# Kernel tuning notes

Hardware: AMD Instinct MI355X
Metric: run time of the kernel (lower is better)

## Reference

```python
import jax, jax.numpy as jnp
import numpy as np

N_NODES = 100000
N_EDGES = 1250000
HID = 64          # structure_hidden_dim
N_RBF = 32
N_GRAPHS = 512
N_EXPERTS = 8
N_LAYERS = 3
CUTOFF = 6.0
MAX_Z = 100
GATE_IN = HID + N_EXPERTS  # 72
G1, G2 = 64, 32            # gate_hidden_dims


def setup_inputs() -> dict:
    key = jax.random.key(0)
    ks = jax.random.split(key, 32)
    s = 0.05
    inp = {
        'z': jax.random.randint(ks[0], (N_NODES,), 0, MAX_Z),
        'edge_index': jax.random.randint(ks[1], (2, N_EDGES), 0, N_NODES),
        'edge_weight': jax.random.uniform(ks[2], (N_EDGES,), dtype=jnp.float32) * CUTOFF,
        'batch': jnp.sort(jax.random.randint(ks[3], (N_NODES,), 0, N_GRAPHS)),
        'mlip_energies': jax.random.normal(ks[4], (N_GRAPHS, N_EXPERTS), dtype=jnp.float32),
        # SchNet parameters (torch nn.Linear convention: W is [out, in])
        'emb': jax.random.normal(ks[5], (MAX_Z, HID)) * s,
        'fW1': jax.random.normal(ks[6], (N_LAYERS, HID, N_RBF)) * s,
        'fb1': jnp.zeros((N_LAYERS, HID)),
        'fW2': jax.random.normal(ks[7], (N_LAYERS, HID, HID)) * s,
        'fb2': jnp.zeros((N_LAYERS, HID)),
        'dW': jax.random.normal(ks[8], (N_LAYERS, HID, HID)) * s,
        'db': jnp.zeros((N_LAYERS, HID)),
        'uW1': jax.random.normal(ks[9], (N_LAYERS, HID, HID)) * s,
        'ub1': jnp.zeros((N_LAYERS, HID)),
        'uW2': jax.random.normal(ks[10], (N_LAYERS, HID, HID)) * s,
        'ub2': jnp.zeros((N_LAYERS, HID)),
        # Gating MLP: (HID+E) -> 64 -> 32 -> E
        'gW1': jax.random.normal(ks[11], (G1, GATE_IN)) * s,
        'gb1': jnp.zeros((G1,)),
        'gW2': jax.random.normal(ks[12], (G2, G1)) * s,
        'gb2': jnp.zeros((G2,)),
        'gW3': jax.random.normal(ks[13], (N_EXPERTS, G2)) * s,
        'gb3': jnp.zeros((N_EXPERTS,)),
    }
    return inp


def reference(z, edge_index, edge_weight, batch, mlip_energies,
              emb, fW1, fb1, fW2, fb2, dW, db, uW1, ub1, uW2, ub2,
              gW1, gb1, gW2, gb2, gW3, gb3):
    src, dst = edge_index[0], edge_index[1]

    # Gaussian smearing of distances -> [E, N_RBF]
    offsets = jnp.linspace(0.0, CUTOFF, N_RBF, dtype=edge_weight.dtype)
    delta = offsets[1] - offsets[0]
    coeff = -0.5 / (delta * delta)
    diff = edge_weight[:, None] - offsets
    edge_attr = jnp.exp(coeff * diff * diff)

    # atom embedding [N, HID]
    x = emb[z]

    for i in range(N_LAYERS):
        # filter network: Linear -> SiLU -> Linear on RBF features [E, HID]
        f = jax.nn.silu(edge_attr @ fW1[i].T + fb1[i]) @ fW2[i].T + fb2[i]
        # gather + dense + elementwise filter -> messages [E, HID]
        msg = (x[src] @ dW[i].T + db[i]) * f
        # scatter-add to destination nodes [N, HID]
        agg = jax.ops.segment_sum(msg, dst, num_segments=N_NODES)
        # residual update MLP
        x = x + (jax.nn.silu(agg @ uW1[i].T + ub1[i]) @ uW2[i].T + ub2[i])

    # mean pool per graph [G, HID]
    pooled = jax.ops.segment_sum(x, batch, num_segments=N_GRAPHS)
    counts = jax.ops.segment_sum(jnp.ones((N_NODES,), x.dtype), batch, num_segments=N_GRAPHS)
    structure_embedding = pooled / jnp.maximum(counts, 1.0)[:, None]

    # gated MoE head
    gate_in = jnp.concatenate([structure_embedding, mlip_energies], axis=-1)
    h = jax.nn.relu(gate_in @ gW1.T + gb1)
    h = jax.nn.relu(h @ gW2.T + gb2)
    logits = h @ gW3.T + gb3
    weights = jax.nn.softmax(logits, axis=-1)
    prediction = jnp.sum(mlip_energies * weights, axis=-1)
    return (logits, weights, prediction)
```

## Files before the change

### kernel.cpp

```cpp
#include <hip/hip_runtime.h>
#include <hip/hip_fp16.h>
#include <math.h>

#define N_NODES   100000
#define N_EDGES   1250000
#define HID       64
#define N_RBF     32
#define N_GRAPHS  512
#define N_EXPERTS 8
#define N_LAYERS  3
#define CUTOFF    6.0f
#define GATE_IN   72
#define G1_DIM    64
#define G2_DIM    32
#define K_TAB     4096
#define N_BUCKET  391
#define BUCKET_CAP 4608
#define CHUNK_A   2048

typedef short short8 __attribute__((ext_vector_type(8)));
typedef float float4v __attribute__((ext_vector_type(4)));

__device__ __forceinline__ unsigned enc8(float v) {
  unsigned short u = __half_as_ushort(__float2half(v));
  return (unsigned)((unsigned short)(u + 0x80u) >> 8);
}
__device__ __forceinline__ float dec8(unsigned b) {
  return __half2float(__ushort_as_half((unsigned short)(b << 8)));
}
__device__ __forceinline__ unsigned short bf16(float f) {
  unsigned u = __float_as_uint(f);
  u += 0x7fffu + ((u >> 16) & 1u);
  return (unsigned short)(u >> 16);
}

__global__ __launch_bounds__(256) void build_tab(
    const float* __restrict__ fW1, const float* __restrict__ fb1,
    const float* __restrict__ fW2, const float* __restrict__ fb2,
    float* __restrict__ tab) {
  __shared__ float W1s[64][33];
  __shared__ float W2s[64][65];
  __shared__ float rbfs[4][32];
  __shared__ float h1s[4][64];
  int t = threadIdx.x;
  int wv = t >> 6, lane = t & 63;
  int layer = blockIdx.x / 1025;
  int k = (blockIdx.x % 1025) * 4 + wv;

  for (int i = t; i < 64 * 32; i += 256) W1s[i >> 5][i & 31] = fW1[layer * 2048 + i];
  for (int i = t; i < 64 * 64; i += 256) W2s[i >> 6][i & 63] = fW2[layer * 4096 + i];

  float w = (CUTOFF / (float)K_TAB) * (float)k;
  const float delta = CUTOFF / (float)(N_RBF - 1);
  const float coeff = -0.5f / (delta * delta);
  __syncthreads();

  if (lane < N_RBF) {
    float d = w - delta * (float)lane;
    rbfs[wv][lane] = expf(coeff * d * d);
  }
  __syncthreads();

  float s = fb1[layer * HID + lane];
#pragma unroll
  for (int j = 0; j < N_RBF; j++) s += rbfs[wv][j] * W1s[lane][j];
  h1s[wv][lane] = s / (1.0f + expf(-s));
  __syncthreads();

  float f = fb2[layer * HID + lane];
#pragma unroll
  for (int c = 0; c < HID; c++) f += h1s[wv][c] * W2s[lane][c];
  if (k <= K_TAB) tab[(layer * (K_TAB + 1) + k) * HID + lane] = f;
}

__global__ __launch_bounds__(256) void pack_tab8(
    const float* __restrict__ tab, unsigned char* __restrict__ tab8) {
  int i = blockIdx.x * 256 + threadIdx.x;
  if (i >= N_LAYERS * K_TAB * 64) return;
  int layer = i / (K_TAB * 64);
  int r = i - layer * (K_TAB * 64);
  const float* base = tab + layer * (K_TAB + 1) * 64;
  tab8[i] = (unsigned char)enc8(0.5f * (base[r] + base[r + 64]));
}

__global__ __launch_bounds__(256) void conv_w(
    const float* __restrict__ dW, const float* __restrict__ uW1,
    const float* __restrict__ uW2, unsigned short* __restrict__ dWh,
    unsigned short* __restrict__ uW1h, unsigned short* __restrict__ uW2h) {
  int i = blockIdx.x * 256 + threadIdx.x;
  if (i < N_LAYERS * 4096) {
    dWh[i]  = bf16(dW[i]);
    uW1h[i] = bf16(uW1[i]);
    uW2h[i] = bf16(uW2[i]);
  }
}

__global__ __launch_bounds__(256) void partitionA(
    const int* __restrict__ src, const int* __restrict__ dst,
    const float* __restrict__ ew, int* __restrict__ gcnt,
    uint2* __restrict__ stage) {
  __shared__ int hist[N_BUCKET];
  __shared__ int base[N_BUCKET];
  int t = threadIdx.x;
  int e0 = blockIdx.x * CHUNK_A;
  int e1 = e0 + CHUNK_A; if (e1 > N_EDGES) e1 = N_EDGES;

  for (int i = t; i < N_BUCKET; i += 256) hist[i] = 0;
  __syncthreads();
  for (int e = e0 + t; e < e1; e += 256)
    atomicAdd(&hist[dst[e] >> 8], 1);
  __syncthreads();
  for (int i = t; i < N_BUCKET; i += 256) {
    int c = hist[i];
    base[i] = c ? atomicAdd(&gcnt[i], c) : 0;
    hist[i] = 0;
  }
  __syncthreads();
  for (int e = e0 + t; e < e1; e += 256) {
    int d = dst[e];
    int b = d >> 8;
    int r = base[b] + atomicAdd(&hist[b], 1);
    if (r < BUCKET_CAP) {
      float uq = ew[e] * ((float)K_TAB / CUTOFF);
      int wq = (int)uq;
      if (wq > K_TAB - 1) wq = K_TAB - 1;
      stage[(size_t)b * BUCKET_CAP + r] =
          make_uint2(((unsigned)src[e] << 12) | (unsigned)wq, (unsigned)d);
    }
  }
}

__global__ __launch_bounds__(512) void bscan_kernel(
    const int* __restrict__ gcnt, int* __restrict__ bbase,
    int* __restrict__ rowstart) {
  __shared__ int sh[512];
  int t = threadIdx.x;
  int v = 0;
  if (t < N_BUCKET) {
    v = gcnt[t];
    if (v > BUCKET_CAP) v = BUCKET_CAP;
  }
  sh[t] = v;
  __syncthreads();
  for (int off = 1; off < 512; off <<= 1) {
    int add = (t >= off) ? sh[t - off] : 0;
    __syncthreads();
    sh[t] += add;
    __syncthreads();
  }
  if (t < N_BUCKET) bbase[t] = sh[t] - v;
  if (t == N_BUCKET - 1) {
    bbase[N_BUCKET] = sh[t];
    rowstart[N_NODES] = sh[t];
  }
}

__global__ __launch_bounds__(512) void sortB(
    const int* __restrict__ bbase, const uint2* __restrict__ stage,
    int* __restrict__ rowstart, unsigned* __restrict__ recs) {
  __shared__ int cnt[256];
  __shared__ int scn[256];
  __shared__ unsigned dest[BUCKET_CAP];
  int t = threadIdx.x;
  int b = blockIdx.x;
  int node0 = b << 8;
  int base = bbase[b];
  int total = bbase[b + 1] - base;
  const uint2* st = stage + (size_t)b * BUCKET_CAP;

  if (t < 256) cnt[t] = 0;
  __syncthreads();
  for (int k = t; k < total; k += 512) atomicAdd(&cnt[(int)st[k].y - node0], 1);
  __syncthreads();
  int v = 0;
  if (t < 256) { v = cnt[t]; scn[t] = v; }
  __syncthreads();
  for (int off = 1; off < 256; off <<= 1) {
    int add = (t < 256 && t >= off) ? scn[t - off] : 0;
    __syncthreads();
    if (t < 256) scn[t] += add;
    __syncthreads();
  }
  if (t < 256) {
    int excl = scn[t] - v;
    int n = node0 + t;
    if (n < N_NODES) rowstart[n] = base + excl;
    scn[t] = excl;
    cnt[t] = 0;
  }
  __syncthreads();
  for (int k = t; k < total; k += 512) {
    uint2 e = st[k];
    int ln = (int)e.y - node0;
    int r = atomicAdd(&cnt[ln], 1);
    dest[scn[ln] + r] = e.x;
  }
  __syncthreads();
  for (int k = t; k < total; k += 512) recs[base + k] = dest[k];
}

__global__ __launch_bounds__(256, 4) void dense0(
    const int* __restrict__ z, const float* __restrict__ emb,
    const unsigned short* __restrict__ Wh,
    const float* __restrict__ b, unsigned char* __restrict__ yb) {
  __shared__ __align__(16) unsigned char smem[18432];
  short* As = (short*)smem;
  short* Bs = As + 64 * 72;
  float* Es = (float*)smem;
  int t = threadIdx.x;
  int row0 = blockIdx.x * 64;

#pragma unroll
  for (int it = 0; it < 4; it++) {
    int i = it * 1024 + t * 4;
    int r = i >> 6, c = i & 63;
    int gr = row0 + r;
    float4 v = make_float4(0.f, 0.f, 0.f, 0.f);
    if (gr < N_NODES) {
      int zi = z[gr];
      v = *(const float4*)&emb[(size_t)zi * 64 + c];
    }
    short4 h;
    h.x = (short)bf16(v.x); h.y = (short)bf16(v.y);
    h.z = (short)bf16(v.z); h.w = (short)bf16(v.w);
    *(short4*)&As[r * 72 + c] = h;
  }
#pragma unroll
  for (int it = 0; it < 2; it++) {
    int i = it * 2048 + t * 8;
    int r = i >> 6, c = i & 63;
    *(uint4*)&Bs[r * 72 + c] = *(const uint4*)&Wh[i];
  }
  __syncthreads();

  int lane = t & 63, wv = t >> 6;
  int m = lane & 15, quad = lane >> 4;
  const short* arow = As + (wv * 16 + m) * 72 + quad * 8;
  short8 a0 = *(const short8*)arow;
  short8 a1 = *(const short8*)(arow + 32);
  float4v acc[4];
#pragma unroll
  for (int ct = 0; ct < 4; ct++) {
    const short* brow = Bs + (ct * 16 + m) * 72 + quad * 8;
    short8 bf0 = *(const short8*)brow;
    short8 bf1 = *(const short8*)(brow + 32);
    float bj = b[ct * 16 + m];
    float4v c = {bj, bj, bj, bj};
    c = __builtin_amdgcn_mfma_f32_16x16x32_bf16(a0, bf0, c, 0, 0, 0);
    c = __builtin_amdgcn_mfma_f32_16x16x32_bf16(a1, bf1, c, 0, 0, 0);
    acc[ct] = c;
  }
  __syncthreads();
#pragma unroll
  for (int ct = 0; ct < 4; ct++)
#pragma unroll
    for (int r = 0; r < 4; r++)
      Es[(wv * 16 + quad * 4 + r) * 68 + ct * 16 + m] = acc[ct][r];
  __syncthreads();
  {
    int row = t >> 2, c0 = (t & 3) * 16;
    int gr = row0 + row;
    if (gr < N_NODES) {
      unsigned w[4];
#pragma unroll
      for (int q = 0; q < 4; q++) {
        const float* p = &Es[row * 68 + c0 + 4 * q];
        w[q] = enc8(p[0]) | (enc8(p[1]) << 8) | (enc8(p[2]) << 16) | (enc8(p[3]) << 24);
      }
      *(uint4*)&yb[(size_t)gr * 64 + c0] = make_uint4(w[0], w[1], w[2], w[3]);
    }
  }
}

__global__ __launch_bounds__(256, 4) void update_dense(
    const unsigned short* __restrict__ aggb,
    const unsigned short* __restrict__ W1h, const float* __restrict__ ub1,
    const unsigned short* __restrict__ W2h, const float* __restrict__ ub2,
    float* __restrict__ x,
    const int* __restrict__ z, const float* __restrict__ emb,
    const unsigned short* __restrict__ dWn, const float* __restrict__ dbn,
    unsigned char* __restrict__ yb) {
  __shared__ __align__(16) short A1[64 * 72];
  __shared__ __align__(16) short B1[64 * 72];
  __shared__ __align__(16) float E[64 * 68];
  int t = threadIdx.x;
  int row0 = blockIdx.x * 64;
  int lane = t & 63, wv = t >> 6;
  int m = lane & 15, quad = lane >> 4;

#pragma unroll
  for (int it = 0; it < 4; it++) {
    int i = it * 1024 + t * 4;
    int r = i >> 6, c = i & 63;
    int gr = row0 + r;
    float4 v = make_float4(0.f, 0.f, 0.f, 0.f);
    if (gr < N_NODES) {
      if (z) {
        int zi = z[gr];
        v = *(const float4*)&emb[(size_t)zi * 64 + c];
      } else {
        v = *(const float4*)&x[(size_t)gr * 64 + c];
      }
    }
    *(float4*)&E[r * 68 + c] = v;
  }
#pragma unroll
  for (int it = 0; it < 2; it++) {
    int i = it * 2048 + t * 8;
    int r = i >> 6, c = i & 63;
    int gr = row0 + r;
    uint4 v = make_uint4(0u, 0u, 0u, 0u);
    if (gr < N_NODES) v = *(const uint4*)&aggb[(size_t)gr * 64 + c];
    *(uint4*)&A1[r * 72 + c] = v;
    *(uint4*)&B1[r * 72 + c] = *(const uint4*)&W1h[i];
  }
  __syncthreads();

  const short* arow = A1 + (wv * 16 + m) * 72 + quad * 8;
  float4v acc[4];
  {
    short8 a0 = *(const short8*)arow;
    short8 a1 = *(const short8*)(arow + 32);
#pragma unroll
    for (int ct = 0; ct < 4; ct++) {
      const short* brow = B1 + (ct * 16 + m) * 72 + quad * 8;
      short8 bf0 = *(const short8*)brow;
      short8 bf1 = *(const short8*)(brow + 32);
      float bj = ub1[ct * 16 + m];
      float4v c = {bj, bj, bj, bj};
      c = __builtin_amdgcn_mfma_f32_16x16x32_bf16(a0, bf0, c, 0, 0, 0);
      c = __builtin_amdgcn_mfma_f32_16x16x32_bf16(a1, bf1, c, 0, 0, 0);
      acc[ct] = c;
    }
  }
  __syncthreads();
#pragma unroll
  for (int ct = 0; ct < 4; ct++)
#pragma unroll
    for (int r = 0; r < 4; r++) {
      float s = acc[ct][r];
      float h = s / (1.0f + expf(-s));
      A1[(wv * 16 + quad * 4 + r) * 72 + ct * 16 + m] = (short)bf16(h);
    }
#pragma unroll
  for (int it = 0; it < 2; it++) {
    int i = it * 2048 + t * 8;
    int r = i >> 6, c = i & 63;
    *(uint4*)&B1[r * 72 + c] = *(const uint4*)&W2h[i];
  }
  __syncthreads();

  {
    short8 a0 = *(const short8*)arow;
    short8 a1 = *(const short8*)(arow + 32);
#pragma unroll
    for (int ct = 0; ct < 4; ct++) {
      const short* brow = B1 + (ct * 16 + m) * 72 + quad * 8;
      short8 bf0 = *(const short8*)brow;
      short8 bf1 = *(const short8*)(brow + 32);
      float bj = ub2[ct * 16 + m];
      float4v c = {bj, bj, bj, bj};
      c = __builtin_amdgcn_mfma_f32_16x16x32_bf16(a0, bf0, c, 0, 0, 0);
      c = __builtin_amdgcn_mfma_f32_16x16x32_bf16(a1, bf1, c, 0, 0, 0);
      acc[ct] = c;
    }
  }
  __syncthreads();
#pragma unroll
  for (int ct = 0; ct < 4; ct++)
#pragma unroll
    for (int r = 0; r < 4; r++)
      E[(wv * 16 + quad * 4 + r) * 68 + ct * 16 + m] += acc[ct][r];
  __syncthreads();
  {
    int row = t >> 2, c0 = (t & 3) * 16;
    int gr = row0 + row;
    if (gr < N_NODES) {
      float* xp = x + (size_t)gr * 64 + c0;
#pragma unroll
      for (int q = 0; q < 4; q++)
        *(float4*)(xp + 4 * q) = *(const float4*)&E[row * 68 + c0 + 4 * q];
    }
  }
  if (!dWn) return;

#pragma unroll
  for (int it = 0; it < 4; it++) {
    int i = it * 1024 + t * 4;
    int r = i >> 6, c = i & 63;
    float4 v = *(const float4*)&E[r * 68 + c];
    short4 h;
    h.x = (short)bf16(v.x); h.y = (short)bf16(v.y);
    h.z = (short)bf16(v.z); h.w = (short)bf16(v.w);
    *(short4*)&A1[r * 72 + c] = h;
  }
#pragma unroll
  for (int it = 0; it < 2; it++) {
    int i = it * 2048 + t * 8;
    int r = i >> 6, c = i & 63;
    *(uint4*)&B1[r * 72 + c] = *(const uint4*)&dWn[i];
  }
  __syncthreads();
  {
    short8 a0 = *(const short8*)arow;
    short8 a1 = *(const short8*)(arow + 32);
#pragma unroll
    for (int ct = 0; ct < 4; ct++) {
      const short* brow = B1 + (ct * 16 + m) * 72 + quad * 8;
      short8 bf0 = *(const short8*)brow;
      short8 bf1 = *(const short8*)(brow + 32);
      float bj = dbn[ct * 16 + m];
      float4v c = {bj, bj, bj, bj};
      c = __builtin_amdgcn_mfma_f32_16x16x32_bf16(a0, bf0, c, 0, 0, 0);
      c = __builtin_amdgcn_mfma_f32_16x16x32_bf16(a1, bf1, c, 0, 0, 0);
      acc[ct] = c;
    }
  }
  __syncthreads();
#pragma unroll
  for (int ct = 0; ct < 4; ct++)
#pragma unroll
    for (int r = 0; r < 4; r++)
      E[(wv * 16 + quad * 4 + r) * 68 + ct * 16 + m] = acc[ct][r];
  __syncthreads();
  {
    int row = t >> 2, c0 = (t & 3) * 16;
    int gr = row0 + row;
    if (gr < N_NODES) {
      unsigned w[4];
#pragma unroll
      for (int q = 0; q < 4; q++) {
        const float* p = &E[row * 68 + c0 + 4 * q];
        w[q] = enc8(p[0]) | (enc8(p[1]) << 8) | (enc8(p[2]) << 16) | (enc8(p[3]) << 24);
      }
      *(uint4*)&yb[(size_t)gr * 64 + c0] = make_uint4(w[0], w[1], w[2], w[3]);
    }
  }
}

__global__ __launch_bounds__(256) void gather_kernel(
    const int* __restrict__ rowstart, const unsigned* __restrict__ recs,
    const unsigned char* __restrict__ tab8,
    const unsigned char* __restrict__ yb,
    unsigned short* __restrict__ aggb) {
  int d = blockIdx.x * 4 + (threadIdx.x >> 6);
  int lane = threadIdx.x & 63;
  int b0 = __builtin_amdgcn_readfirstlane(rowstart[d]);
  int b1 = __builtin_amdgcn_readfirstlane(rowstart[d + 1]);
  float acc = 0.0f;
  int j = b0;
  for (; j + 4 <= b1; j += 4) {
    unsigned u0 = recs[j];
    unsigned u1 = recs[j + 1];
    unsigned u2 = recs[j + 2];
    unsigned u3 = recs[j + 3];
    unsigned y0 = yb[((u0 >> 12) << 6) + lane];
    unsigned y1 = yb[((u1 >> 12) << 6) + lane];
    unsigned y2 = yb[((u2 >> 12) << 6) + lane];
    unsigned y3 = yb[((u3 >> 12) << 6) + lane];
    unsigned f0 = tab8[((u0 & 4095u) << 6) + lane];
    unsigned f1 = tab8[((u1 & 4095u) << 6) + lane];
    unsigned f2 = tab8[((u2 & 4095u) << 6) + lane];
    unsigned f3 = tab8[((u3 & 4095u) << 6) + lane];
    acc += dec8(y0) * dec8(f0);
    acc += dec8(y1) * dec8(f1);
    acc += dec8(y2) * dec8(f2);
    acc += dec8(y3) * dec8(f3);
  }
  for (; j < b1; j++) {
    unsigned u = recs[j];
    unsigned yv = yb[((u >> 12) << 6) + lane];
    unsigned fv = tab8[((u & 4095u) << 6) + lane];
    acc += dec8(yv) * dec8(fv);
  }
  aggb[(size_t)d * 64 + lane] = bf16(acc);
}

__global__ __launch_bounds__(256) void pool_kernel(
    const float* __restrict__ x, const int* __restrict__ batch,
    float* __restrict__ pooled, float* __restrict__ counts) {
  int wid = (blockIdx.x * 256 + threadIdx.x) >> 6;
  int lane = threadIdx.x & 63;
  int n0 = wid * 64;
  if (n0 >= N_NODES) return;
  int n1 = n0 + 64; if (n1 > N_NODES) n1 = N_NODES;
  int curg = batch[n0];
  float acc = 0.0f, cnt = 0.0f;
  for (int n = n0; n < n1; n++) {
    int g = batch[n];
    if (g != curg) {
      unsafeAtomicAdd(&pooled[curg * 64 + lane], acc);
      if (lane == 0) unsafeAtomicAdd(&counts[curg], cnt);
      curg = g; acc = 0.0f; cnt = 0.0f;
    }
    acc += x[n * 64 + lane];
    cnt += 1.0f;
  }
  unsafeAtomicAdd(&pooled[curg * 64 + lane], acc);
  if (lane == 0) unsafeAtomicAdd(&counts[curg], cnt);
}

__global__ __launch_bounds__(256) void gate_kernel(
    const float* __restrict__ pooled, const float* __restrict__ counts,
    const float* __restrict__ mlip,
    const float* __restrict__ gW1, const float* __restrict__ gb1,
    const float* __restrict__ gW2, const float* __restrict__ gb2,
    const float* __restrict__ gW3, const float* __restrict__ gb3,
    float* __restrict__ out) {
  __shared__ float ins[4][GATE_IN];
  __shared__ float h1s[4][G1_DIM];
  __shared__ float h2s[4][G2_DIM];
  __shared__ float lg[4][N_EXPERTS];
  int wv = threadIdx.x >> 6, lane = threadIdx.x & 63;
  int g = blockIdx.x * 4 + wv;

  float cnt = counts[g];
  if (cnt < 1.0f) cnt = 1.0f;
  ins[wv][lane] = pooled[g * 64 + lane] / cnt;
  if (lane < N_EXPERTS) ins[wv][64 + lane] = mlip[g * N_EXPERTS + lane];
  __syncthreads();

  {
    float s = gb1[lane];
    for (int c = 0; c < GATE_IN; c++) s += ins[wv][c] * gW1[lane * GATE_IN + c];
    h1s[wv][lane] = fmaxf(s, 0.0f);
  }
  __syncthreads();
  if (lane < G2_DIM) {
    float s = gb2[lane];
    for (int c = 0; c < G1_DIM; c++) s += h1s[wv][c] * gW2[lane * G1_DIM + c];
    h2s[wv][lane] = fmaxf(s, 0.0f);
  }
  __syncthreads();
  if (lane < N_EXPERTS) {
    float s = gb3[lane];
    for (int c = 0; c < G2_DIM; c++) s += h2s[wv][c] * gW3[lane * G2_DIM + c];
    lg[wv][lane] = s;
  }
  __syncthreads();
  if (lane < N_EXPERTS) {
    float m = -1e30f;
    for (int j = 0; j < N_EXPERTS; j++) m = fmaxf(m, lg[wv][j]);
    float den = 0.0f;
    for (int j = 0; j < N_EXPERTS; j++) den += expf(lg[wv][j] - m);
    float wgt = expf(lg[wv][lane] - m) / den;
    out[g * 8 + lane] = lg[wv][lane];
    out[N_GRAPHS * 8 + g * 8 + lane] = wgt;
    if (lane == 0) {
      float p = 0.0f;
      for (int j = 0; j < N_EXPERTS; j++)
        p += mlip[g * 8 + j] * expf(lg[wv][j] - m) / den;
      out[N_GRAPHS * 16 + g] = p;
    }
  }
}

extern "C" void kernel_launch(void* const* d_in, const int* in_sizes, int n_in,
                              void* d_out, int out_size, void* d_ws, size_t ws_size,
                              hipStream_t stream) {
  const int*   z     = (const int*)  d_in[0];
  const int*   ei    = (const int*)  d_in[1];
  const float* ew    = (const float*)d_in[2];
  const int*   batch = (const int*)  d_in[3];
  const float* mlip  = (const float*)d_in[4];
  const float* emb   = (const float*)d_in[5];
  const float* fW1   = (const float*)d_in[6];
  const float* fb1   = (const float*)d_in[7];
  const float* fW2   = (const float*)d_in[8];
  const float* fb2   = (const float*)d_in[9];
  const float* dW    = (const float*)d_in[10];
  const float* db    = (const float*)d_in[11];
  const float* uW1   = (const float*)d_in[12];
  const float* ub1   = (const float*)d_in[13];
  const float* uW2   = (const float*)d_in[14];
  const float* ub2   = (const float*)d_in[15];
  const float* gW1   = (const float*)d_in[16];
  const float* gb1   = (const float*)d_in[17];
  const float* gW2   = (const float*)d_in[18];
  const float* gb2   = (const float*)d_in[19];
  const float* gW3   = (const float*)d_in[20];
  const float* gb3   = (const float*)d_in[21];

  const int* src = ei;
  const int* dst = ei + N_EDGES;

  float* ws = (float*)d_ws;
  float*          x        = ws;
  unsigned char*  yb       = (unsigned char*)(ws + 6400000);
  unsigned short* aggb     = (unsigned short*)(ws + 8000000);
  float*          tab      = ws + 11200000;
  unsigned char*  tab8     = (unsigned char*)(ws + 11986624);
  float*          pooled   = ws + 12183232;
  float*          counts   = ws + 12216000;
  int*            rowstart = (int*)(ws + 12216512);
  unsigned*       recs     = (unsigned*)(ws + 12316513);
  int*            gcnt     = (int*)(ws + 13566513);
  int*            bbase    = (int*)(ws + 13566904);
  uint2*          stage    = (uint2*)(ws + 13567296);
  unsigned short* dWh      = (unsigned short*)(ws + 17171008);
  unsigned short* uW1h     = dWh + N_LAYERS * 4096;
  unsigned short* uW2h     = uW1h + N_LAYERS * 4096;

  hipMemsetAsync(gcnt, 0, N_BUCKET * sizeof(int), stream);
  partitionA<<<(N_EDGES + CHUNK_A - 1) / CHUNK_A, 256, 0, stream>>>(
      src, dst, ew, gcnt, stage);
  bscan_kernel<<<1, 512, 0, stream>>>(gcnt, bbase, rowstart);
  sortB<<<N_BUCKET, 512, 0, stream>>>(bbase, stage, rowstart, recs);

  build_tab<<<N_LAYERS * 1025, 256, 0, stream>>>(fW1, fb1, fW2, fb2, tab);
  pack_tab8<<<(N_LAYERS * K_TAB * 64) / 256, 256, 0, stream>>>(tab, tab8);
  conv_w<<<(N_LAYERS * 4096 + 255) / 256, 256, 0, stream>>>(dW, uW1, uW2, dWh, uW1h, uW2h);

  const int NBLK = (N_NODES + 63) / 64;
  dense0<<<NBLK, 256, 0, stream>>>(z, emb, dWh, db, yb);

  gather_kernel<<<N_NODES / 4, 256, 0, stream>>>(rowstart, recs, tab8, yb, aggb);
  update_dense<<<NBLK, 256, 0, stream>>>(aggb, uW1h, ub1, uW2h, ub2, x,
                                         z, emb, dWh + 4096, db + 64, yb);
  gather_kernel<<<N_NODES / 4, 256, 0, stream>>>(rowstart, recs, tab8 + K_TAB * 64, yb, aggb);
  update_dense<<<NBLK, 256, 0, stream>>>(aggb, uW1h + 4096, ub1 + 64, uW2h + 4096, ub2 + 64, x,
                                         nullptr, nullptr, dWh + 8192, db + 128, yb);
  gather_kernel<<<N_NODES / 4, 256, 0, stream>>>(rowstart, recs, tab8 + 2 * K_TAB * 64, yb, aggb);
  update_dense<<<NBLK, 256, 0, stream>>>(aggb, uW1h + 8192, ub1 + 128, uW2h + 8192, ub2 + 128, x,
                                         nullptr, nullptr, nullptr, nullptr, nullptr);

  hipMemsetAsync(pooled, 0, (size_t)(N_GRAPHS * HID + N_GRAPHS) * sizeof(float), stream);
  pool_kernel<<<(N_NODES / 64 + 1 + 3) / 4, 256, 0, stream>>>(x, batch, pooled, counts);
  gate_kernel<<<N_GRAPHS / 4, 256, 0, stream>>>(pooled, counts, mlip,
                                                gW1, gb1, gW2, gb2, gW3, gb3,
                                                (float*)d_out);
}
```

Before: 395.3 us.

## Fuse prep kernels and memsets into one launch, fold pooling into last update

Merges the filter-table build, the 8-bit table packing and the weight bf16 conversion into a single prep kernel. The same kernel also zeroes the bucket counters and pooled buffers, so both memsets go away. The table is now sampled at bin midpoints directly instead of averaging two fp32 endpoints, which removes the intermediate fp32 table. The last update_dense does the per-graph mean-pool atomics straight from shared memory and skips writing x, which removes the separate pool kernel and its re-read of x.

```diff
diff --git a/kernel.cpp b/kernel.cpp
--- a/kernel.cpp
+++ b/kernel.cpp
@@ -34,23 +34,41 @@
   return (unsigned short)(u >> 16);
 }
 
-__global__ __launch_bounds__(256) void build_tab(
+__global__ __launch_bounds__(256) void prep_kernel(
     const float* __restrict__ fW1, const float* __restrict__ fb1,
     const float* __restrict__ fW2, const float* __restrict__ fb2,
-    float* __restrict__ tab) {
+    const float* __restrict__ dW, const float* __restrict__ uW1,
+    const float* __restrict__ uW2,
+    unsigned char* __restrict__ tab8,
+    unsigned short* __restrict__ dWh, unsigned short* __restrict__ uW1h,
+    unsigned short* __restrict__ uW2h,
+    int* __restrict__ gcnt, float* __restrict__ pooled) {
+  int b = blockIdx.x;
+  int t = threadIdx.x;
+  if (b >= N_LAYERS * 1024) {
+    if (b < N_LAYERS * 1024 + 48) {
+      int i = (b - N_LAYERS * 1024) * 256 + t;
+      dWh[i]  = bf16(dW[i]);
+      uW1h[i] = bf16(uW1[i]);
+      uW2h[i] = bf16(uW2[i]);
+    } else {
+      for (int i = t; i < N_BUCKET; i += 256) gcnt[i] = 0;
+      for (int i = t; i < N_GRAPHS * HID + N_GRAPHS; i += 256) pooled[i] = 0.0f;
+    }
+    return;
+  }
   __shared__ float W1s[64][33];
   __shared__ float W2s[64][65];
   __shared__ float rbfs[4][32];
   __shared__ float h1s[4][64];
-  int t = threadIdx.x;
   int wv = t >> 6, lane = t & 63;
-  int layer = blockIdx.x / 1025;
-  int k = (blockIdx.x % 1025) * 4 + wv;
+  int layer = b >> 10;
+  int k = (b & 1023) * 4 + wv;
 
   for (int i = t; i < 64 * 32; i += 256) W1s[i >> 5][i & 31] = fW1[layer * 2048 + i];
   for (int i = t; i < 64 * 64; i += 256) W2s[i >> 6][i & 63] = fW2[layer * 4096 + i];
 
-  float w = (CUTOFF / (float)K_TAB) * (float)k;
+  float w = ((float)k + 0.5f) * (CUTOFF / (float)K_TAB);
   const float delta = CUTOFF / (float)(N_RBF - 1);
   const float coeff = -0.5f / (delta * delta);
   __syncthreads();
@@ -70,29 +88,7 @@
   float f = fb2[layer * HID + lane];
 #pragma unroll
   for (int c = 0; c < HID; c++) f += h1s[wv][c] * W2s[lane][c];
-  if (k <= K_TAB) tab[(layer * (K_TAB + 1) + k) * HID + lane] = f;
-}
-
-__global__ __launch_bounds__(256) void pack_tab8(
-    const float* __restrict__ tab, unsigned char* __restrict__ tab8) {
-  int i = blockIdx.x * 256 + threadIdx.x;
-  if (i >= N_LAYERS * K_TAB * 64) return;
-  int layer = i / (K_TAB * 64);
-  int r = i - layer * (K_TAB * 64);
-  const float* base = tab + layer * (K_TAB + 1) * 64;
-  tab8[i] = (unsigned char)enc8(0.5f * (base[r] + base[r + 64]));
-}
-
-__global__ __launch_bounds__(256) void conv_w(
-    const float* __restrict__ dW, const float* __restrict__ uW1,
-    const float* __restrict__ uW2, unsigned short* __restrict__ dWh,
-    unsigned short* __restrict__ uW1h, unsigned short* __restrict__ uW2h) {
-  int i = blockIdx.x * 256 + threadIdx.x;
-  if (i < N_LAYERS * 4096) {
-    dWh[i]  = bf16(dW[i]);
-    uW1h[i] = bf16(uW1[i]);
-    uW2h[i] = bf16(uW2[i]);
-  }
+  tab8[(layer * K_TAB + k) * HID + lane] = (unsigned char)enc8(f);
 }
 
 __global__ __launch_bounds__(256) void partitionA(
@@ -279,7 +275,9 @@
     float* __restrict__ x,
     const int* __restrict__ z, const float* __restrict__ emb,
     const unsigned short* __restrict__ dWn, const float* __restrict__ dbn,
-    unsigned char* __restrict__ yb) {
+    unsigned char* __restrict__ yb,
+    const int* __restrict__ batch, float* __restrict__ pooled,
+    float* __restrict__ counts) {
   __shared__ __align__(16) short A1[64 * 72];
   __shared__ __align__(16) short B1[64 * 72];
   __shared__ __align__(16) float E[64 * 68];
@@ -372,6 +370,32 @@
     for (int r = 0; r < 4; r++)
       E[(wv * 16 + quad * 4 + r) * 68 + ct * 16 + m] += acc[ct][r];
   __syncthreads();
+
+  if (batch) {
+    int curg = -1;
+    float accv = 0.0f, cntv = 0.0f;
+    for (int i = 0; i < 16; i++) {
+      int r = wv * 16 + i;
+      int gr = row0 + r;
+      if (gr >= N_NODES) break;
+      int g = batch[gr];
+      if (g != curg) {
+        if (curg >= 0) {
+          unsafeAtomicAdd(&pooled[curg * 64 + lane], accv);
+          if (lane == 0) unsafeAtomicAdd(&counts[curg], cntv);
+        }
+        curg = g; accv = 0.0f; cntv = 0.0f;
+      }
+      accv += E[r * 68 + lane];
+      cntv += 1.0f;
+    }
+    if (curg >= 0) {
+      unsafeAtomicAdd(&pooled[curg * 64 + lane], accv);
+      if (lane == 0) unsafeAtomicAdd(&counts[curg], cntv);
+    }
+    return;
+  }
+
   {
     int row = t >> 2, c0 = (t & 3) * 16;
     int gr = row0 + row;
@@ -476,30 +500,6 @@
   aggb[(size_t)d * 64 + lane] = bf16(acc);
 }
 
-__global__ __launch_bounds__(256) void pool_kernel(
-    const float* __restrict__ x, const int* __restrict__ batch,
-    float* __restrict__ pooled, float* __restrict__ counts) {
-  int wid = (blockIdx.x * 256 + threadIdx.x) >> 6;
-  int lane = threadIdx.x & 63;
-  int n0 = wid * 64;
-  if (n0 >= N_NODES) return;
-  int n1 = n0 + 64; if (n1 > N_NODES) n1 = N_NODES;
-  int curg = batch[n0];
-  float acc = 0.0f, cnt = 0.0f;
-  for (int n = n0; n < n1; n++) {
-    int g = batch[n];
-    if (g != curg) {
-      unsafeAtomicAdd(&pooled[curg * 64 + lane], acc);
-      if (lane == 0) unsafeAtomicAdd(&counts[curg], cnt);
-      curg = g; acc = 0.0f; cnt = 0.0f;
-    }
-    acc += x[n * 64 + lane];
-    cnt += 1.0f;
-  }
-  unsafeAtomicAdd(&pooled[curg * 64 + lane], acc);
-  if (lane == 0) unsafeAtomicAdd(&counts[curg], cnt);
-}
-
 __global__ __launch_bounds__(256) void gate_kernel(
     const float* __restrict__ pooled, const float* __restrict__ counts,
     const float* __restrict__ mlip,
@@ -588,44 +588,42 @@
   float*          x        = ws;
   unsigned char*  yb       = (unsigned char*)(ws + 6400000);
   unsigned short* aggb     = (unsigned short*)(ws + 8000000);
-  float*          tab      = ws + 11200000;
-  unsigned char*  tab8     = (unsigned char*)(ws + 11986624);
-  float*          pooled   = ws + 12183232;
-  float*          counts   = ws + 12216000;
-  int*            rowstart = (int*)(ws + 12216512);
-  unsigned*       recs     = (unsigned*)(ws + 12316513);
-  int*            gcnt     = (int*)(ws + 13566513);
-  int*            bbase    = (int*)(ws + 13566904);
-  uint2*          stage    = (uint2*)(ws + 13567296);
-  unsigned short* dWh      = (unsigned short*)(ws + 17171008);
+  unsigned char*  tab8     = (unsigned char*)(ws + 11200000);
+  int*            rowstart = (int*)(ws + 11396608);
+  unsigned*       recs     = (unsigned*)(ws + 11496609);
+  int*            gcnt     = (int*)(ws + 12746609);
+  int*            bbase    = (int*)(ws + 12747000);
+  uint2*          stage    = (uint2*)(ws + 12747392);
+  unsigned short* dWh      = (unsigned short*)(ws + 16350848);
   unsigned short* uW1h     = dWh + N_LAYERS * 4096;
   unsigned short* uW2h     = uW1h + N_LAYERS * 4096;
-
-  hipMemsetAsync(gcnt, 0, N_BUCKET * sizeof(int), stream);
+  float*          pooled   = ws + 16369280;
+  float*          counts   = ws + 16402048;
+
+  prep_kernel<<<N_LAYERS * 1024 + 49, 256, 0, stream>>>(
+      fW1, fb1, fW2, fb2, dW, uW1, uW2, tab8, dWh, uW1h, uW2h, gcnt, pooled);
+
   partitionA<<<(N_EDGES + CHUNK_A - 1) / CHUNK_A, 256, 0, stream>>>(
       src, dst, ew, gcnt, stage);
   bscan_kernel<<<1, 512, 0, stream>>>(gcnt, bbase, rowstart);
   sortB<<<N_BUCKET, 512, 0, stream>>>(bbase, stage, rowstart, recs);
 
-  build_tab<<<N_LAYERS * 1025, 256, 0, stream>>>(fW1, fb1, fW2, fb2, tab);
-  pack_tab8<<<(N_LAYERS * K_TAB * 64) / 256, 256, 0, stream>>>(tab, tab8);
-  conv_w<<<(N_LAYERS * 4096 + 255) / 256, 256, 0, stream>>>(dW, uW1, uW2, dWh, uW1h, uW2h);
-
   const int NBLK = (N_NODES + 63) / 64;
   dense0<<<NBLK, 256, 0, stream>>>(z, emb, dWh, db, yb);
 
   gather_kernel<<<N_NODES / 4, 256, 0, stream>>>(rowstart, recs, tab8, yb, aggb);
   update_dense<<<NBLK, 256, 0, stream>>>(aggb, uW1h, ub1, uW2h, ub2, x,
-                                         z, emb, dWh + 4096, db + 64, yb);
+                                         z, emb, dWh + 4096, db + 64, yb,
+                                         nullptr, nullptr, nullptr);
   gather_kernel<<<N_NODES / 4, 256, 0, stream>>>(rowstart, recs, tab8 + K_TAB * 64, yb, aggb);
   update_dense<<<NBLK, 256, 0, stream>>>(aggb, uW1h + 4096, ub1 + 64, uW2h + 4096, ub2 + 64, x,
-                                         nullptr, nullptr, dWh + 8192, db + 128, yb);
+                                         nullptr, nullptr, dWh + 8192, db + 128, yb,
+                                         nullptr, nullptr, nullptr);
   gather_kernel<<<N_NODES / 4, 256, 0, stream>>>(rowstart, recs, tab8 + 2 * K_TAB * 64, yb, aggb);
   update_dense<<<NBLK, 256, 0, stream>>>(aggb, uW1h + 8192, ub1 + 128, uW2h + 8192, ub2 + 128, x,
-                                         nullptr, nullptr, nullptr, nullptr, nullptr);
-
-  hipMemsetAsync(pooled, 0, (size_t)(N_GRAPHS * HID + N_GRAPHS) * sizeof(float), stream);
-  pool_kernel<<<(N_NODES / 64 + 1 + 3) / 4, 256, 0, stream>>>(x, batch, pooled, counts);
+                                         nullptr, nullptr, nullptr, nullptr, nullptr,
+                                         batch, pooled, counts);
+
   gate_kernel<<<N_GRAPHS / 4, 256, 0, stream>>>(pooled, counts, mlip,
                                                 gW1, gb1, gW2, gb2, gW3, gb3,
                                                 (float*)d_out);
```

Result: faster. 369.8 us (-6.5%).
